# Kernel optimization log

Hardware: AMD Instinct MI355X
Metric: run time of the kernel (lower is better)

Reference implementation:

```python
import jax, jax.numpy as jnp
import numpy as np

# Dimensions (match init_kwargs / input_specs)
B, S, DIN = 8, 128, 768
N, D, H = 64, 128, 4          # num_slots, slot_dim, num_heads
DH = D // H
MAX_TICKS = 8
THR = 0.5
EPS = 1e-5


def setup_inputs() -> dict:
    key = jax.random.key(0)
    ks = jax.random.split(key, 16)
    init = lambda k, shape: (jax.random.normal(k, shape) * 0.02).astype(jnp.float32)
    return {
        "x": jax.random.normal(ks[0], (B, S, DIN), dtype=jnp.float32),
        "slot_memory": init(ks[1], (1, N, D)),
        "ln_w": jnp.ones((DIN,), jnp.float32),
        "ln_b": jnp.zeros((DIN,), jnp.float32),
        "w_in": init(ks[2], (DIN, D)),
        "w_q": init(ks[3], (D, D)),
        "w_k": init(ks[4], (D, D)),
        "w_v": init(ks[5], (D, D)),
        "w_gate": init(ks[6], (D, N)),
        "b_gate": jnp.zeros((N,), jnp.float32),
        "halt_w1": init(ks[7], (D, D // 2)),
        "halt_b1": jnp.zeros((D // 2,), jnp.float32),
        "halt_w2": init(ks[8], (D // 2, 1)),
        "halt_b2": jnp.zeros((1,), jnp.float32),
        "w_out": init(ks[9], (D, DIN)),
        "dn_wk": init(ks[10], (D, D)),
        "dn_wv": init(ks[11], (D, D)),
        "dn_wb": init(ks[12], (D, H)),
        "dn_bb": jnp.zeros((H,), jnp.float32),
        "dn_lam": jnp.full((D,), 0.9, dtype=jnp.float32),
        "dn_wo": init(ks[13], (D, D)),
    }


def _layernorm(x, w, b):
    mu = jnp.mean(x, axis=-1, keepdims=True)
    var = jnp.mean((x - mu) ** 2, axis=-1, keepdims=True)
    return (x - mu) * jax.lax.rsqrt(var + EPS) * w + b


def _deltanet(read_out, slots, dn_wk, dn_wv, dn_wb, dn_bb, dn_lam, dn_wo):
    # Delta-rule cell, vectorized over all N slots at once (same input, per-slot state).
    k = (read_out @ dn_wk).reshape(B, 1, H, DH)
    k = k / (jnp.linalg.norm(k, axis=-1, keepdims=True) + 1e-6)
    v = (read_out @ dn_wv).reshape(B, 1, H, DH)
    # beta in (0,2) -> allows negative eigenvalues of (I - beta k k^T)
    beta = (2.0 * jax.nn.sigmoid(read_out @ dn_wb + dn_bb))[:, None, :, None]
    h = slots.reshape(B, N, H, DH)
    kh = jnp.sum(k * h, axis=-1, keepdims=True)           # (B,N,H,1)
    lam = dn_lam.reshape(1, 1, H, DH)
    h_new = lam * h + beta * (v - kh * k)                 # delta-rule update
    return h_new.reshape(B, N, D) @ dn_wo


def reference(x, slot_memory, ln_w, ln_b, w_in, w_q, w_k, w_v, w_gate, b_gate,
              halt_w1, halt_b1, halt_w2, halt_b2, w_out,
              dn_wk, dn_wv, dn_wb, dn_bb, dn_lam, dn_wo):
    slots0 = jnp.broadcast_to(slot_memory, (B, N, D)).astype(x.dtype)
    scale = jnp.sqrt(jnp.asarray(D, x.dtype))

    def seq_step(slots, x_t):
        x_proj = _layernorm(x_t, ln_w, ln_b) @ w_in       # (B,D)

        def tick(carry, t):
            slots, acc, rem, active = carry
            # attention read
            q = x_proj @ w_q
            kk = slots @ w_k
            vv = slots @ w_v
            attn = jax.nn.softmax(jnp.einsum('bd,bnd->bn', q, kk) / scale, axis=-1)
            read_out = jnp.einsum('bn,bnd->bd', attn, vv)
            # halting + write gate
            halt = jax.nn.sigmoid(jax.nn.relu(read_out @ halt_w1 + halt_b1) @ halt_w2 + halt_b2)  # (B,1)
            gate = jax.nn.sigmoid(read_out @ w_gate + b_gate)[..., None]  # (B,N,1)
            upd = _deltanet(read_out, slots, dn_wk, dn_wv, dn_wb, dn_bb, dn_lam, dn_wo)
            new_slots = (1.0 - gate) * slots + gate * upd
            acc2 = acc + rem * read_out
            rem2 = jnp.where(t < MAX_TICKS - 1, rem * (1.0 - halt), rem)
            # apply this tick only if not yet halted (emulates torch break)
            slots = jnp.where(active, new_slots, slots)
            acc = jnp.where(active, acc2, acc)
            rem = jnp.where(active, rem2, rem)
            active2 = active & jnp.logical_not((jnp.mean(halt) > THR) & (t > 0))
            return (slots, acc, rem, active2), None

        acc0 = jnp.zeros((B, D), x.dtype)
        rem0 = jnp.ones((B, 1), x.dtype)
        (slots, acc, _, _), _ = jax.lax.scan(
            tick, (slots, acc0, rem0, jnp.array(True)), jnp.arange(MAX_TICKS))
        return slots, acc @ w_out

    slots_final, outs = jax.lax.scan(seq_step, slots0, jnp.swapaxes(x, 0, 1))
    return jnp.swapaxes(outs, 0, 1), slots_final
```

## Files before the change

kernel.cpp:

```cpp
#include <hip/hip_runtime.h>
#include <cstdint>

#define TB 8
#define TS 128
#define TDIN 768
#define TN 64
#define TD 128
#define TH 4
#define TMAXT 8

#define WS_WLAM 0
#define WS_M    16384
#define WS_QK   32768
#define WS_ACC  163840
#define WS_HALT 294912
#define WS_C    491520
#define WS_BW   557056

__device__ __forceinline__ float wsum64(float v) {
  v += __shfl_xor(v, 1);  v += __shfl_xor(v, 2);  v += __shfl_xor(v, 4);
  v += __shfl_xor(v, 8);  v += __shfl_xor(v, 16); v += __shfl_xor(v, 32);
  return v;
}
__device__ __forceinline__ float wmax64(float v) {
  v = fmaxf(v, __shfl_xor(v, 1));  v = fmaxf(v, __shfl_xor(v, 2));
  v = fmaxf(v, __shfl_xor(v, 4));  v = fmaxf(v, __shfl_xor(v, 8));
  v = fmaxf(v, __shfl_xor(v, 16)); v = fmaxf(v, __shfl_xor(v, 32));
  return v;
}

__global__ __launch_bounds__(256) void k0_prep(const float* __restrict__ w_q,
                                               const float* __restrict__ w_k,
                                               const float* __restrict__ dn_lam,
                                               const float* __restrict__ dn_wo,
                                               float* __restrict__ ws) {
  const int bx = blockIdx.x, tid = threadIdx.x;
  if (bx < 32) {
    int i = bx * 512 + tid;
    ws[WS_WLAM + i] = dn_lam[i >> 7] * dn_wo[i];
    i += 256;
    ws[WS_WLAM + i] = dn_lam[i >> 7] * dn_wo[i];
  } else {
    __shared__ float part[2][128];
    const int r0 = (bx - 32) * 4;
    const int c = tid & 127, half = tid >> 7;
    for (int rr = 0; rr < 4; ++rr) {
      const int k = r0 + rr;
      const float* wq = w_q + k * TD + half * 64;
      const float* wk = w_k + c * TD + half * 64;
      float p = 0.f;
      #pragma unroll 8
      for (int d = 0; d < 64; ++d) p = fmaf(wq[d], wk[d], p);
      part[half][c] = p;
      __syncthreads();
      if (tid < 128) ws[WS_M + k * TD + tid] = part[0][tid] + part[1][tid];
      __syncthreads();
    }
  }
}

__device__ __forceinline__ float k0c_dot(const float* __restrict__ row,
                                         const float* __restrict__ Wcol, int stride) {
  float sAcc = 0.f;
  #pragma unroll 8
  for (int m = 0; m < TD; ++m) sAcc = fmaf(row[m], Wcol[m * stride], sAcc);
  return sAcc;
}

__global__ __launch_bounds__(256) void k0c_prep(const float* __restrict__ w_v,
                                                const float* __restrict__ dn_wk,
                                                const float* __restrict__ dn_wv,
                                                const float* __restrict__ w_gate,
                                                const float* __restrict__ halt_w1,
                                                const float* __restrict__ dn_wb,
                                                float* __restrict__ ws) {
  const int k = blockIdx.x, tid = threadIdx.x;
  __shared__ float row[TD];
  if (tid < TD) row[tid] = w_v[k * TD + tid];
  __syncthreads();
  float* Crow = ws + WS_C + (size_t)k * 512;
  #pragma unroll
  for (int pass = 0; pass < 2; ++pass) {
    const int c = tid + pass * 256;
    float val;
    if (c < 128)       val = row[c];
    else if (c < 256)  val = k0c_dot(row, dn_wk + (c - 128), TD);
    else if (c < 384)  val = k0c_dot(row, dn_wv + (c - 256), TD);
    else if (c < 448)  val = k0c_dot(row, w_gate + (c - 384), TN);
    else               val = k0c_dot(row, halt_w1 + (c - 448), 64);
    Crow[c] = val;
  }
  if (tid < 4) ws[WS_BW + k * TH + tid] = k0c_dot(row, dn_wb + tid, TH);
}

__global__ __launch_bounds__(256) void k1_qk(const float* __restrict__ x,
                                             const float* __restrict__ ln_w,
                                             const float* __restrict__ ln_b,
                                             const float* __restrict__ w_in,
                                             float* __restrict__ ws) {
  const int bx = blockIdx.x, tid = threadIdx.x;
  const int b = bx >> 5;
  const int s0 = (bx & 31) * 4;
  const int wv = tid >> 6, lane = tid & 63;

  __shared__ float xn[4][TDIN];
  __shared__ float xp[4][TD];
  __shared__ float part[2][4][TD];
  __shared__ float red[4];

  for (int ss = 0; ss < 4; ++ss) {
    const float* xrow = x + ((size_t)(b * TS + s0 + ss)) * TDIN;
    float v0 = xrow[tid], v1 = xrow[tid + 256], v2 = xrow[tid + 512];
    float p = wsum64(v0 + v1 + v2);
    if (lane == 0) red[wv] = p;
    __syncthreads();
    const float mu = (red[0] + red[1] + red[2] + red[3]) * (1.f / 768.f);
    __syncthreads();
    const float d0 = v0 - mu, d1 = v1 - mu, d2 = v2 - mu;
    p = wsum64(d0 * d0 + d1 * d1 + d2 * d2);
    if (lane == 0) red[wv] = p;
    __syncthreads();
    const float var = (red[0] + red[1] + red[2] + red[3]) * (1.f / 768.f);
    const float rstd = 1.f / sqrtf(var + 1e-5f);
    xn[ss][tid]       = d0 * rstd * ln_w[tid]       + ln_b[tid];
    xn[ss][tid + 256] = d1 * rstd * ln_w[tid + 256] + ln_b[tid + 256];
    xn[ss][tid + 512] = d2 * rstd * ln_w[tid + 512] + ln_b[tid + 512];
    __syncthreads();
  }

  {
    const int d = tid & 127, j = tid >> 7;
    float a0 = 0.f, a1 = 0.f, a2 = 0.f, a3 = 0.f;
    const int kb = j * 384;
    #pragma unroll 4
    for (int k = 0; k < 384; ++k) {
      const float w = w_in[(kb + k) * TD + d];
      a0 = fmaf(xn[0][kb + k], w, a0);
      a1 = fmaf(xn[1][kb + k], w, a1);
      a2 = fmaf(xn[2][kb + k], w, a2);
      a3 = fmaf(xn[3][kb + k], w, a3);
    }
    part[j][0][d] = a0; part[j][1][d] = a1; part[j][2][d] = a2; part[j][3][d] = a3;
  }
  __syncthreads();
  if (tid < 128) {
    #pragma unroll
    for (int ss = 0; ss < 4; ++ss) xp[ss][tid] = part[0][ss][tid] + part[1][ss][tid];
  }
  __syncthreads();
  {
    const int c = tid & 127, j = tid >> 7;
    float a0 = 0.f, a1 = 0.f, a2 = 0.f, a3 = 0.f;
    const float* Mp = ws + WS_M;
    const int kb = j * 64;
    #pragma unroll 4
    for (int k = 0; k < 64; ++k) {
      const float m = Mp[(kb + k) * TD + c];
      a0 = fmaf(xp[0][kb + k], m, a0);
      a1 = fmaf(xp[1][kb + k], m, a1);
      a2 = fmaf(xp[2][kb + k], m, a2);
      a3 = fmaf(xp[3][kb + k], m, a3);
    }
    part[j][0][c] = a0; part[j][1][c] = a1; part[j][2][c] = a2; part[j][3][c] = a3;
  }
  __syncthreads();
  if (tid < 128) {
    #pragma unroll
    for (int ss = 0; ss < 4; ++ss)
      ws[WS_QK + (size_t)(b * TS + s0 + ss) * TD + tid] = part[0][ss][tid] + part[1][ss][tid];
  }
}


template<int C0, int NC>
__device__ __forceinline__ void gemm_lds(const float* __restrict__ shW,
                                         const float (*S)[129], int l, float* G) {
  #pragma unroll
  for (int j = 0; j < NC; ++j) G[j] = 0.f;
  #pragma unroll 4
  for (int k = 0; k < 128; ++k) {
    const float a = S[l][k];
    const float4* wrow = (const float4*)(&shW[k * TD + C0]);
    #pragma unroll
    for (int jq = 0; jq < NC / 4; ++jq) {
      const float4 w = wrow[jq];
      G[4*jq+0] = fmaf(a, w.x, G[4*jq+0]);
      G[4*jq+1] = fmaf(a, w.y, G[4*jq+1]);
      G[4*jq+2] = fmaf(a, w.z, G[4*jq+2]);
      G[4*jq+3] = fmaf(a, w.w, G[4*jq+3]);
    }
  }
}

template<int C0, int NC>
__device__ __forceinline__ float score_cols(const float (*S)[129], int l,
                                            const float* sh_qk) {
  float sp = 0.f;
  #pragma unroll
  for (int jq = 0; jq < NC / 4; ++jq) {
    const int c = C0 + 4 * jq;
    const float4 qv = *(const float4*)(&sh_qk[c]);
    sp = fmaf(S[l][c+0], qv.x, sp);
    sp = fmaf(S[l][c+1], qv.y, sp);
    sp = fmaf(S[l][c+2], qv.z, sp);
    sp = fmaf(S[l][c+3], qv.w, sp);
  }
  return sp;
}

template<int C0, int NC>
__device__ __forceinline__ float commit_cols(float (*S)[129], int l, const float* G,
                                             float g, float kh0, float kh1, float kh2, float kh3,
                                             const float (*sh_vo)[TD], const float (*sh_ko)[TD],
                                             const float* sh_qk) {
  float sp = 0.f;
  const float omg = 1.f - g;
  #pragma unroll
  for (int jq = 0; jq < NC / 4; ++jq) {
    const int c = C0 + 4 * jq;
    const float4 v0 = *(const float4*)(&sh_vo[0][c]);
    const float4 v1 = *(const float4*)(&sh_vo[1][c]);
    const float4 v2 = *(const float4*)(&sh_vo[2][c]);
    const float4 v3 = *(const float4*)(&sh_vo[3][c]);
    const float4 k0 = *(const float4*)(&sh_ko[0][c]);
    const float4 k1 = *(const float4*)(&sh_ko[1][c]);
    const float4 k2 = *(const float4*)(&sh_ko[2][c]);
    const float4 k3 = *(const float4*)(&sh_ko[3][c]);
    const float4 qv = *(const float4*)(&sh_qk[c]);
    float u;
    u = G[4*jq+0] + (v0.x - kh0*k0.x) + (v1.x - kh1*k1.x) + (v2.x - kh2*k2.x) + (v3.x - kh3*k3.x);
    { const float ns = omg * S[l][c+0] + g * u; S[l][c+0] = ns; sp = fmaf(ns, qv.x, sp); }
    u = G[4*jq+1] + (v0.y - kh0*k0.y) + (v1.y - kh1*k1.y) + (v2.y - kh2*k2.y) + (v3.y - kh3*k3.y);
    { const float ns = omg * S[l][c+1] + g * u; S[l][c+1] = ns; sp = fmaf(ns, qv.y, sp); }
    u = G[4*jq+2] + (v0.z - kh0*k0.z) + (v1.z - kh1*k1.z) + (v2.z - kh2*k2.z) + (v3.z - kh3*k3.z);
    { const float ns = omg * S[l][c+2] + g * u; S[l][c+2] = ns; sp = fmaf(ns, qv.z, sp); }
    u = G[4*jq+3] + (v0.w - kh0*k0.w) + (v1.w - kh1*k1.w) + (v2.w - kh2*k2.w) + (v3.w - kh3*k3.w);
    { const float ns = omg * S[l][c+3] + g * u; S[l][c+3] = ns; sp = fmaf(ns, qv.w, sp); }
  }
  return sp;
}

template<int C0, int NC>
__device__ __forceinline__ void store_cols(const float (*S)[129], int l,
                                           float* __restrict__ dst) {
  #pragma unroll
  for (int j = 0; j < NC; ++j) dst[l * TD + C0 + j] = S[l][C0 + j];
}

__global__ __launch_bounds__(512, 1) void k2_main(
    const float* __restrict__ slot_memory,
    const float* __restrict__ b_gate,
    const float* __restrict__ halt_b1, const float* __restrict__ halt_w2,
    const float* __restrict__ halt_b2,
    const float* __restrict__ dn_bb,   const float* __restrict__ dn_wo,
    float* __restrict__ ws, float* __restrict__ out) {
  const int tid = threadIdx.x;
  const int b = blockIdx.x;
  const int l = tid & 63, wv = tid >> 6;

  __shared__ float shW[TD * TD];
  __shared__ float S[TN][129];
  __shared__ float sh_scorepart[8][TN];
  __shared__ float sh_qk[TD];
  __shared__ float sh_rs[TD];
  __shared__ float sh_ro[TD];
  __shared__ float sh_gate[TN];
  __shared__ float sh_kn[TD];
  __shared__ float sh_v[TD];
  __shared__ float sh_beta[TH];
  __shared__ float sh_vo[TH][TD];
  __shared__ float sh_ko[TH][TD];
  __shared__ float sh_kh[TH][TN];
  __shared__ float sh_bw[TD * TH];
  __shared__ float sh_hb1[64], sh_hw2[64], sh_bg[64], sh_bb[TH];
  __shared__ float sh_hl, sh_hb2;
  __shared__ int   sh_break;

  unsigned long long* hslots = (unsigned long long*)(ws + WS_HALT);

  for (int i = tid; i < TD * TD; i += 512) shW[i] = ws[WS_WLAM + i];
  for (int i = tid; i < TN * TD; i += 512) S[i >> 7][i & 127] = slot_memory[i];
  for (int i = tid; i < TD * TH; i += 512) sh_bw[i] = ws[WS_BW + i];
  if (tid < 64) { sh_hb1[tid] = halt_b1[tid]; sh_hw2[tid] = halt_w2[tid]; sh_bg[tid] = b_gate[tid]; }
  if (tid < TH) sh_bb[tid] = dn_bb[tid];
  if (tid == 0) sh_hb2 = halt_b2[0];

  float creg[128];
  {
    const float* cp = ws + WS_C + tid;
    #pragma unroll
    for (int k = 0; k < 128; ++k) creg[k] = cp[k * 512];
  }
  float wo_reg[32];
  {
    const int h = tid >> 7, c = tid & 127;
    const float* wp = dn_wo + (h * 32) * TD + c;
    #pragma unroll
    for (int i = 0; i < 32; ++i) wo_reg[i] = wp[i * TD];
  }
  __syncthreads();

  float acc0 = 0.f, acc1 = 0.f, rem = 1.f;

  for (int s = 0; s < TS; ++s) {
    if (tid < TD) sh_qk[tid] = ws[WS_QK + (size_t)(b * TS + s) * TD + tid];
    if (wv == 0) { acc0 = 0.f; acc1 = 0.f; rem = 1.f; }
    __syncthreads();
    {
      float sp = 0.f;
      switch (wv) {
        case 1: sp = score_cols<0, 20>(S, l, sh_qk); break;
        case 2: sp = score_cols<20, 20>(S, l, sh_qk); break;
        case 3: sp = score_cols<40, 20>(S, l, sh_qk); break;
        case 4: sp = score_cols<60, 16>(S, l, sh_qk); break;
        case 5: sp = score_cols<76, 16>(S, l, sh_qk); break;
        case 6: sp = score_cols<92, 16>(S, l, sh_qk); break;
        case 7: sp = score_cols<108, 20>(S, l, sh_qk); break;
        default: break;
      }
      if (wv) sh_scorepart[wv][l] = sp;
    }
    __syncthreads();

    for (int t = 0; t < TMAXT; ++t) {
      float G[20];
      if (wv == 0) {
        float sc = sh_scorepart[1][l] + sh_scorepart[2][l] + sh_scorepart[3][l]
                 + sh_scorepart[4][l] + sh_scorepart[5][l] + sh_scorepart[6][l]
                 + sh_scorepart[7][l];
        const float y = sc * 0.08838834764831845f;
        const float mx = wmax64(y);
        const float e = expf(y - mx);
        const float se = wsum64(e);
        const float a = e / se;
        float r0 = 0.f, r1 = 0.f;
        #pragma unroll 8
        for (int n = 0; n < TN; ++n) {
          const float an = __shfl(a, n);
          r0 = fmaf(an, S[n][l], r0);
          r1 = fmaf(an, S[n][l + 64], r1);
        }
        sh_rs[l] = r0; sh_rs[l + 64] = r1;
        if (t >= 2) {
          if (l < 8) {
            const unsigned want = (unsigned)(s * 8 + t - 1);
            const size_t ei = ((size_t)(s * 6 + t - 2) * 8 + l) * 16;
            unsigned long long vv_ =
                __hip_atomic_load(&hslots[ei], __ATOMIC_RELAXED, __HIP_MEMORY_SCOPE_AGENT);
            while ((unsigned)(vv_ >> 32) != want) {
              __builtin_amdgcn_s_sleep(1);
              vv_ = __hip_atomic_load(&hslots[ei], __ATOMIC_RELAXED, __HIP_MEMORY_SCOPE_AGENT);
            }
            float hv = __uint_as_float((unsigned)vv_);
            hv += __shfl_xor(hv, 1); hv += __shfl_xor(hv, 2); hv += __shfl_xor(hv, 4);
            if (l == 0) sh_break = (hv * 0.125f > 0.5f) ? 1 : 0;
          }
        } else if (l == 0) {
          sh_break = 0;
        }
      } else {
        switch (wv) {
          case 1: gemm_lds<0, 20>(shW, S, l, G); break;
          case 2: gemm_lds<20, 20>(shW, S, l, G); break;
          case 3: gemm_lds<40, 20>(shW, S, l, G); break;
          case 4: gemm_lds<60, 16>(shW, S, l, G); break;
          case 5: gemm_lds<76, 16>(shW, S, l, G); break;
          case 6: gemm_lds<92, 16>(shW, S, l, G); break;
          default: gemm_lds<108, 20>(shW, S, l, G); break;
        }
      }
      __syncthreads();
      if (sh_break) break;

      {
        float a0 = 0.f, a1 = 0.f, a2 = 0.f, a3 = 0.f;
        #pragma unroll
        for (int kq = 0; kq < 32; ++kq) {
          const float4 r4 = *(const float4*)(&sh_rs[4 * kq]);
          a0 = fmaf(r4.x, creg[4*kq+0], a0);
          a1 = fmaf(r4.y, creg[4*kq+1], a1);
          a2 = fmaf(r4.z, creg[4*kq+2], a2);
          a3 = fmaf(r4.w, creg[4*kq+3], a3);
        }
        const float acc = (a0 + a1) + (a2 + a3);
        if (wv == 0) {
          sh_ro[l] = acc;
          if (l < 4) {
            float bacc = 0.f;
            #pragma unroll 8
            for (int k = 0; k < 128; ++k) bacc = fmaf(sh_rs[k], sh_bw[k * TH + l], bacc);
            sh_beta[l] = 2.f / (1.f + expf(-(bacc + sh_bb[l])));
          }
        } else if (wv == 1) {
          sh_ro[64 + l] = acc;
        } else if (wv == 2 || wv == 3) {
          const int d = (wv - 2) * 64 + l;
          float sq = acc * acc;
          sq += __shfl_xor(sq, 1); sq += __shfl_xor(sq, 2); sq += __shfl_xor(sq, 4);
          sq += __shfl_xor(sq, 8); sq += __shfl_xor(sq, 16);
          sh_kn[d] = acc / (sqrtf(sq) + 1e-6f);
        } else if (wv == 4) {
          sh_v[l] = acc;
        } else if (wv == 5) {
          sh_v[64 + l] = acc;
        } else if (wv == 6) {
          sh_gate[l] = 1.f / (1.f + expf(-(acc + sh_bg[l])));
        } else {
          const float t1 = fmaxf(acc + sh_hb1[l], 0.f);
          const float z = wsum64(t1 * sh_hw2[l]);
          if (l == 0) {
            const float hlv = 1.f / (1.f + expf(-(z + sh_hb2)));
            sh_hl = hlv;
            if (t >= 1 && t <= 6) {
              const unsigned stamp = (unsigned)(s * 8 + t);
              const size_t ei = ((size_t)(s * 6 + t - 1) * 8 + b) * 16;
              const unsigned long long pv =
                  ((unsigned long long)stamp << 32) | (unsigned long long)__float_as_uint(hlv);
              __hip_atomic_store(&hslots[ei], pv,
                                 __ATOMIC_RELAXED, __HIP_MEMORY_SCOPE_AGENT);
            }
          }
        }
      }
      __syncthreads();

      {
        const int h = tid >> 7;
        const float bh = sh_beta[h];
        float av = 0.f, ak = 0.f;
        #pragma unroll
        for (int iq = 0; iq < 8; ++iq) {
          const float4 vvv = *(const float4*)(&sh_v[h * 32 + 4 * iq]);
          const float4 kkk = *(const float4*)(&sh_kn[h * 32 + 4 * iq]);
          av = fmaf(vvv.x, wo_reg[4*iq+0], av);
          av = fmaf(vvv.y, wo_reg[4*iq+1], av);
          av = fmaf(vvv.z, wo_reg[4*iq+2], av);
          av = fmaf(vvv.w, wo_reg[4*iq+3], av);
          ak = fmaf(kkk.x, wo_reg[4*iq+0], ak);
          ak = fmaf(kkk.y, wo_reg[4*iq+1], ak);
          ak = fmaf(kkk.z, wo_reg[4*iq+2], ak);
          ak = fmaf(kkk.w, wo_reg[4*iq+3], ak);
        }
        const int c = tid & 127;
        sh_vo[h][c] = bh * av;
        sh_ko[h][c] = bh * ak;
        if (tid < 256) {
          const int n = l, hh = wv;
          float kk2 = 0.f;
          #pragma unroll
          for (int iq = 0; iq < 8; ++iq) {
            const float4 kv = *(const float4*)(&sh_kn[hh * 32 + 4 * iq]);
            kk2 = fmaf(kv.x, S[n][hh * 32 + 4 * iq + 0], kk2);
            kk2 = fmaf(kv.y, S[n][hh * 32 + 4 * iq + 1], kk2);
            kk2 = fmaf(kv.z, S[n][hh * 32 + 4 * iq + 2], kk2);
            kk2 = fmaf(kv.w, S[n][hh * 32 + 4 * iq + 3], kk2);
          }
          sh_kh[hh][n] = kk2;
        }
      }
      __syncthreads();

      {
        const float g = sh_gate[l];
        const float kh0 = sh_kh[0][l], kh1 = sh_kh[1][l], kh2 = sh_kh[2][l], kh3 = sh_kh[3][l];
        float sp = 0.f;
        switch (wv) {
          case 1: sp = commit_cols<0, 20>(S, l, G, g, kh0, kh1, kh2, kh3, sh_vo, sh_ko, sh_qk); break;
          case 2: sp = commit_cols<20, 20>(S, l, G, g, kh0, kh1, kh2, kh3, sh_vo, sh_ko, sh_qk); break;
          case 3: sp = commit_cols<40, 20>(S, l, G, g, kh0, kh1, kh2, kh3, sh_vo, sh_ko, sh_qk); break;
          case 4: sp = commit_cols<60, 16>(S, l, G, g, kh0, kh1, kh2, kh3, sh_vo, sh_ko, sh_qk); break;
          case 5: sp = commit_cols<76, 16>(S, l, G, g, kh0, kh1, kh2, kh3, sh_vo, sh_ko, sh_qk); break;
          case 6: sp = commit_cols<92, 16>(S, l, G, g, kh0, kh1, kh2, kh3, sh_vo, sh_ko, sh_qk); break;
          case 7: sp = commit_cols<108, 20>(S, l, G, g, kh0, kh1, kh2, kh3, sh_vo, sh_ko, sh_qk); break;
          default: break;
        }
        if (wv) {
          sh_scorepart[wv][l] = sp;
        } else {
          acc0 += rem * sh_ro[l];
          acc1 += rem * sh_ro[l + 64];
          if (t < TMAXT - 1) rem *= (1.f - sh_hl);
        }
      }
      __syncthreads();
    }

    if (wv == 0) {
      ws[WS_ACC + (size_t)(b * TS + s) * TD + l] = acc0;
      ws[WS_ACC + (size_t)(b * TS + s) * TD + l + 64] = acc1;
    }
  }

  {
    float* dst = out + (size_t)TB * TS * TDIN + (size_t)b * TN * TD;
    switch (wv) {
      case 1: store_cols<0, 20>(S, l, dst); break;
      case 2: store_cols<20, 20>(S, l, dst); break;
      case 3: store_cols<40, 20>(S, l, dst); break;
      case 4: store_cols<60, 16>(S, l, dst); break;
      case 5: store_cols<76, 16>(S, l, dst); break;
      case 6: store_cols<92, 16>(S, l, dst); break;
      case 7: store_cols<108, 20>(S, l, dst); break;
      default: break;
    }
  }
}

__global__ __launch_bounds__(256) void k3_out(const float* __restrict__ w_out,
                                              const float* __restrict__ ws,
                                              float* __restrict__ out) {
  const int bx = blockIdx.x, tid = threadIdx.x;
  const int r0 = bx * 8;
  __shared__ float a8[8][TD];
  for (int i = tid; i < 8 * TD; i += 256)
    a8[i >> 7][i & 127] = ws[WS_ACC + (size_t)r0 * TD + i];
  __syncthreads();
  float p[8][3];
  #pragma unroll
  for (int ss = 0; ss < 8; ++ss) { p[ss][0] = 0.f; p[ss][1] = 0.f; p[ss][2] = 0.f; }
  #pragma unroll 2
  for (int d = 0; d < TD; ++d) {
    const float w0 = w_out[d * TDIN + tid];
    const float w1 = w_out[d * TDIN + tid + 256];
    const float w2 = w_out[d * TDIN + tid + 512];
    #pragma unroll
    for (int ss = 0; ss < 8; ++ss) {
      const float a = a8[ss][d];
      p[ss][0] = fmaf(a, w0, p[ss][0]);
      p[ss][1] = fmaf(a, w1, p[ss][1]);
      p[ss][2] = fmaf(a, w2, p[ss][2]);
    }
  }
  #pragma unroll
  for (int ss = 0; ss < 8; ++ss) {
    out[(size_t)(r0 + ss) * TDIN + tid]       = p[ss][0];
    out[(size_t)(r0 + ss) * TDIN + tid + 256] = p[ss][1];
    out[(size_t)(r0 + ss) * TDIN + tid + 512] = p[ss][2];
  }
}

extern "C" void kernel_launch(void* const* d_in, const int* in_sizes, int n_in,
                              void* d_out, int out_size, void* d_ws, size_t ws_size,
                              hipStream_t stream) {
  (void)in_sizes; (void)n_in; (void)out_size; (void)ws_size;
  const float* x           = (const float*)d_in[0];
  const float* slot_memory = (const float*)d_in[1];
  const float* ln_w        = (const float*)d_in[2];
  const float* ln_b        = (const float*)d_in[3];
  const float* w_in        = (const float*)d_in[4];
  const float* w_q         = (const float*)d_in[5];
  const float* w_k         = (const float*)d_in[6];
  const float* w_v         = (const float*)d_in[7];
  const float* w_gate      = (const float*)d_in[8];
  const float* b_gate      = (const float*)d_in[9];
  const float* halt_w1     = (const float*)d_in[10];
  const float* halt_b1     = (const float*)d_in[11];
  const float* halt_w2     = (const float*)d_in[12];
  const float* halt_b2     = (const float*)d_in[13];
  const float* w_out       = (const float*)d_in[14];
  const float* dn_wk       = (const float*)d_in[15];
  const float* dn_wv       = (const float*)d_in[16];
  const float* dn_wb       = (const float*)d_in[17];
  const float* dn_bb       = (const float*)d_in[18];
  const float* dn_lam      = (const float*)d_in[19];
  const float* dn_wo       = (const float*)d_in[20];
  float* ws  = (float*)d_ws;
  float* out = (float*)d_out;

  k0_prep<<<dim3(64), dim3(256), 0, stream>>>(w_q, w_k, dn_lam, dn_wo, ws);
  k0c_prep<<<dim3(128), dim3(256), 0, stream>>>(w_v, dn_wk, dn_wv, w_gate, halt_w1, dn_wb, ws);
  k1_qk<<<dim3(256), dim3(256), 0, stream>>>(x, ln_w, ln_b, w_in, ws);
  k2_main<<<dim3(TB), dim3(512), 0, stream>>>(slot_memory, b_gate,
                                              halt_b1, halt_w2, halt_b2,
                                              dn_bb, dn_wo, ws, out);
  k3_out<<<dim3(128), dim3(256), 0, stream>>>(w_out, ws, out);
}
```

Baseline: 27.72 ms.

## Speculate past cross-block halt check with slot snapshots and rollback

Instead of spin-waiting for the cross-block mean-halt flag at each tick, the kernel reads it without blocking and keeps computing speculatively. When the flag is not yet available it saves a global snapshot of the slots, and it resolves the real break tick after the tick loop. If the speculation ran too far it restores the snapshot and rebuilds the halting accumulator from the saved per-tick read-outs and halt values. The column split between waves is also changed, with one wave taking 32 columns. This trades the stall latency for extra snapshot traffic and possibly wasted ticks, and it adds LDS and register pressure.

Result: slower. 39.96 ms (+44.1%).

```diff
diff --git a/kernel.cpp b/kernel.cpp
--- a/kernel.cpp
+++ b/kernel.cpp
@@ -16,6 +16,7 @@
 #define WS_HALT 294912
 #define WS_C    491520
 #define WS_BW   557056
+#define WS_SNAP 557568
 
 __device__ __forceinline__ float wsum64(float v) {
   v += __shfl_xor(v, 1);  v += __shfl_xor(v, 2);  v += __shfl_xor(v, 4);
@@ -274,7 +275,11 @@
   __shared__ float sh_bw[TD * TH];
   __shared__ float sh_hb1[64], sh_hw2[64], sh_bg[64], sh_bb[TH];
   __shared__ float sh_hl, sh_hb2;
+  __shared__ float sh_rohist[TMAXT][TD];
+  __shared__ float sh_hlhist[TMAXT];
   __shared__ int   sh_break;
+  __shared__ int   sh_vok;
+  __shared__ int   sh_tb;
 
   unsigned long long* hslots = (unsigned long long*)(ws + WS_HALT);
 
@@ -300,30 +305,30 @@
   }
   __syncthreads();
 
-  float acc0 = 0.f, acc1 = 0.f, rem = 1.f;
-
   for (int s = 0; s < TS; ++s) {
     if (tid < TD) sh_qk[tid] = ws[WS_QK + (size_t)(b * TS + s) * TD + tid];
-    if (wv == 0) { acc0 = 0.f; acc1 = 0.f; rem = 1.f; }
     __syncthreads();
     {
       float sp = 0.f;
       switch (wv) {
-        case 1: sp = score_cols<0, 20>(S, l, sh_qk); break;
-        case 2: sp = score_cols<20, 20>(S, l, sh_qk); break;
-        case 3: sp = score_cols<40, 20>(S, l, sh_qk); break;
-        case 4: sp = score_cols<60, 16>(S, l, sh_qk); break;
-        case 5: sp = score_cols<76, 16>(S, l, sh_qk); break;
-        case 6: sp = score_cols<92, 16>(S, l, sh_qk); break;
-        case 7: sp = score_cols<108, 20>(S, l, sh_qk); break;
+        case 1: sp = score_cols<0, 16>(S, l, sh_qk); break;
+        case 2: sp = score_cols<16, 16>(S, l, sh_qk); break;
+        case 3: sp = score_cols<32, 16>(S, l, sh_qk); break;
+        case 4: sp = score_cols<48, 32>(S, l, sh_qk); break;
+        case 5: sp = score_cols<80, 16>(S, l, sh_qk); break;
+        case 6: sp = score_cols<96, 16>(S, l, sh_qk); break;
+        case 7: sp = score_cols<112, 16>(S, l, sh_qk); break;
         default: break;
       }
       if (wv) sh_scorepart[wv][l] = sp;
     }
     __syncthreads();
 
+    int applied = TMAXT - 1;
+    int vnext = 1;
+
     for (int t = 0; t < TMAXT; ++t) {
-      float G[20];
+      float G[32];
       if (wv == 0) {
         float sc = sh_scorepart[1][l] + sh_scorepart[2][l] + sh_scorepart[3][l]
                  + sh_scorepart[4][l] + sh_scorepart[5][l] + sh_scorepart[6][l]
@@ -342,35 +347,50 @@
         }
         sh_rs[l] = r0; sh_rs[l + 64] = r1;
         if (t >= 2) {
+          int ok = 1; float hv = 0.f;
           if (l < 8) {
             const unsigned want = (unsigned)(s * 8 + t - 1);
             const size_t ei = ((size_t)(s * 6 + t - 2) * 8 + l) * 16;
-            unsigned long long vv_ =
+            const unsigned long long vv =
                 __hip_atomic_load(&hslots[ei], __ATOMIC_RELAXED, __HIP_MEMORY_SCOPE_AGENT);
-            while ((unsigned)(vv_ >> 32) != want) {
-              __builtin_amdgcn_s_sleep(1);
-              vv_ = __hip_atomic_load(&hslots[ei], __ATOMIC_RELAXED, __HIP_MEMORY_SCOPE_AGENT);
-            }
-            float hv = __uint_as_float((unsigned)vv_);
-            hv += __shfl_xor(hv, 1); hv += __shfl_xor(hv, 2); hv += __shfl_xor(hv, 4);
-            if (l == 0) sh_break = (hv * 0.125f > 0.5f) ? 1 : 0;
+            ok = ((unsigned)(vv >> 32) == want) ? 1 : 0;
+            hv = ok ? __uint_as_float((unsigned)vv) : 0.f;
+          }
+          const unsigned long long bal = __ballot(ok);
+          hv += __shfl_xor(hv, 1); hv += __shfl_xor(hv, 2); hv += __shfl_xor(hv, 4);
+          if (l == 0) {
+            const bool allok = ((bal & 0xFFull) == 0xFFull);
+            const bool brk = allok && (hv * 0.125f > 0.5f);
+            sh_break = brk ? 1 : 0;
+            sh_vok = (allok && !brk) ? 1 : 0;
+            if (allok && !brk && vnext == t - 1) vnext = t;
           }
         } else if (l == 0) {
           sh_break = 0;
+          sh_vok = 0;
         }
       } else {
         switch (wv) {
-          case 1: gemm_lds<0, 20>(shW, S, l, G); break;
-          case 2: gemm_lds<20, 20>(shW, S, l, G); break;
-          case 3: gemm_lds<40, 20>(shW, S, l, G); break;
-          case 4: gemm_lds<60, 16>(shW, S, l, G); break;
-          case 5: gemm_lds<76, 16>(shW, S, l, G); break;
-          case 6: gemm_lds<92, 16>(shW, S, l, G); break;
-          default: gemm_lds<108, 20>(shW, S, l, G); break;
+          case 1: gemm_lds<0, 16>(shW, S, l, G); break;
+          case 2: gemm_lds<16, 16>(shW, S, l, G); break;
+          case 3: gemm_lds<32, 16>(shW, S, l, G); break;
+          case 4: gemm_lds<48, 32>(shW, S, l, G); break;
+          case 5: gemm_lds<80, 16>(shW, S, l, G); break;
+          case 6: gemm_lds<96, 16>(shW, S, l, G); break;
+          default: gemm_lds<112, 16>(shW, S, l, G); break;
         }
       }
       __syncthreads();
-      if (sh_break) break;
+      if (sh_break) { applied = t - 1; break; }
+
+      if (t >= 2 && !sh_vok) {
+        float* dst = ws + WS_SNAP + ((size_t)b * 6 + (t - 2)) * 8192;
+        #pragma unroll
+        for (int j = 0; j < 16; ++j) {
+          const int idx = tid + j * 512;
+          dst[idx] = S[idx >> 7][idx & 127];
+        }
+      }
 
       {
         float a0 = 0.f, a1 = 0.f, a2 = 0.f, a3 = 0.f;
@@ -457,6 +477,8 @@
           }
           sh_kh[hh][n] = kk2;
         }
+        if (tid < TD) sh_rohist[t][tid] = sh_ro[tid];
+        if (tid == 0) sh_hlhist[t] = sh_hl;
       }
       __syncthreads();
 
@@ -465,42 +487,80 @@
         const float kh0 = sh_kh[0][l], kh1 = sh_kh[1][l], kh2 = sh_kh[2][l], kh3 = sh_kh[3][l];
         float sp = 0.f;
         switch (wv) {
-          case 1: sp = commit_cols<0, 20>(S, l, G, g, kh0, kh1, kh2, kh3, sh_vo, sh_ko, sh_qk); break;
-          case 2: sp = commit_cols<20, 20>(S, l, G, g, kh0, kh1, kh2, kh3, sh_vo, sh_ko, sh_qk); break;
-          case 3: sp = commit_cols<40, 20>(S, l, G, g, kh0, kh1, kh2, kh3, sh_vo, sh_ko, sh_qk); break;
-          case 4: sp = commit_cols<60, 16>(S, l, G, g, kh0, kh1, kh2, kh3, sh_vo, sh_ko, sh_qk); break;
-          case 5: sp = commit_cols<76, 16>(S, l, G, g, kh0, kh1, kh2, kh3, sh_vo, sh_ko, sh_qk); break;
-          case 6: sp = commit_cols<92, 16>(S, l, G, g, kh0, kh1, kh2, kh3, sh_vo, sh_ko, sh_qk); break;
-          case 7: sp = commit_cols<108, 20>(S, l, G, g, kh0, kh1, kh2, kh3, sh_vo, sh_ko, sh_qk); break;
+          case 1: sp = commit_cols<0, 16>(S, l, G, g, kh0, kh1, kh2, kh3, sh_vo, sh_ko, sh_qk); break;
+          case 2: sp = commit_cols<16, 16>(S, l, G, g, kh0, kh1, kh2, kh3, sh_vo, sh_ko, sh_qk); break;
+          case 3: sp = commit_cols<32, 16>(S, l, G, g, kh0, kh1, kh2, kh3, sh_vo, sh_ko, sh_qk); break;
+          case 4: sp = commit_cols<48, 32>(S, l, G, g, kh0, kh1, kh2, kh3, sh_vo, sh_ko, sh_qk); break;
+          case 5: sp = commit_cols<80, 16>(S, l, G, g, kh0, kh1, kh2, kh3, sh_vo, sh_ko, sh_qk); break;
+          case 6: sp = commit_cols<96, 16>(S, l, G, g, kh0, kh1, kh2, kh3, sh_vo, sh_ko, sh_qk); break;
+          case 7: sp = commit_cols<112, 16>(S, l, G, g, kh0, kh1, kh2, kh3, sh_vo, sh_ko, sh_qk); break;
           default: break;
         }
-        if (wv) {
-          sh_scorepart[wv][l] = sp;
-        } else {
-          acc0 += rem * sh_ro[l];
-          acc1 += rem * sh_ro[l + 64];
-          if (t < TMAXT - 1) rem *= (1.f - sh_hl);
-        }
+        if (wv) sh_scorepart[wv][l] = sp;
       }
       __syncthreads();
     }
 
     if (wv == 0) {
-      ws[WS_ACC + (size_t)(b * TS + s) * TD + l] = acc0;
-      ws[WS_ACC + (size_t)(b * TS + s) * TD + l + 64] = acc1;
-    }
+      int tb = TMAXT - 1;
+      const int v0 = __shfl(vnext, 0);
+      for (int tau = v0; tau <= 6; ++tau) {
+        float hv = 0.f;
+        if (l < 8) {
+          const unsigned want = (unsigned)(s * 8 + tau);
+          const size_t ei = ((size_t)(s * 6 + tau - 1) * 8 + l) * 16;
+          unsigned long long vv =
+              __hip_atomic_load(&hslots[ei], __ATOMIC_RELAXED, __HIP_MEMORY_SCOPE_AGENT);
+          while ((unsigned)(vv >> 32) != want) {
+            __builtin_amdgcn_s_sleep(2);
+            vv = __hip_atomic_load(&hslots[ei], __ATOMIC_RELAXED, __HIP_MEMORY_SCOPE_AGENT);
+          }
+          hv = __uint_as_float((unsigned)vv);
+        }
+        hv += __shfl_xor(hv, 1); hv += __shfl_xor(hv, 2); hv += __shfl_xor(hv, 4);
+        const int brk = (__shfl(hv, 0) * 0.125f > 0.5f) ? 1 : 0;
+        if (brk) { tb = tau; break; }
+      }
+      if (l == 0) sh_tb = tb;
+    }
+    __syncthreads();
+    const int tb = sh_tb;
+    const int napply = (tb < applied) ? tb : applied;
+
+    if (tb < applied) {
+      const float* src = ws + WS_SNAP + ((size_t)b * 6 + (tb - 1)) * 8192;
+      #pragma unroll
+      for (int j = 0; j < 16; ++j) {
+        const int idx = tid + j * 512;
+        S[idx >> 7][idx & 127] = src[idx];
+      }
+    }
+    if (wv == 0) {
+      float rem = 1.f, a0 = 0.f, a1 = 0.f;
+      #pragma unroll
+      for (int t2 = 0; t2 < TMAXT; ++t2) {
+        if (t2 <= napply) {
+          a0 += rem * sh_rohist[t2][l];
+          a1 += rem * sh_rohist[t2][l + 64];
+          if (t2 < TMAXT - 1) rem *= (1.f - sh_hlhist[t2]);
+        }
+      }
+      ws[WS_ACC + (size_t)(b * TS + s) * TD + l] = a0;
+      ws[WS_ACC + (size_t)(b * TS + s) * TD + l + 64] = a1;
+    }
+    __syncthreads();
   }
 
   {
     float* dst = out + (size_t)TB * TS * TDIN + (size_t)b * TN * TD;
     switch (wv) {
-      case 1: store_cols<0, 20>(S, l, dst); break;
-      case 2: store_cols<20, 20>(S, l, dst); break;
-      case 3: store_cols<40, 20>(S, l, dst); break;
-      case 4: store_cols<60, 16>(S, l, dst); break;
-      case 5: store_cols<76, 16>(S, l, dst); break;
-      case 6: store_cols<92, 16>(S, l, dst); break;
-      case 7: store_cols<108, 20>(S, l, dst); break;
+      case 1: store_cols<0, 16>(S, l, dst); break;
+      case 2: store_cols<16, 16>(S, l, dst); break;
+      case 3: store_cols<32, 16>(S, l, dst); break;
+      case 4: store_cols<48, 32>(S, l, dst); break;
+      case 5: store_cols<80, 16>(S, l, dst); break;
+      case 6: store_cols<96, 16>(S, l, dst); break;
+      case 7: store_cols<112, 16>(S, l, dst); break;
       default: break;
     }
   }
```
